# Performance work log

Hardware: AMD Instinct MI355X
Metric: run time of the kernel (lower is better)

## Reference

```python
import jax, jax.numpy as jnp
import numpy as np

D_ATOM, D_PAIR, D_HID = 128, 64, 32
NF, NLOC = 1, 384


def setup_inputs() -> dict:
    key = jax.random.key(0)
    k1, k2, k3, k4, k5 = jax.random.split(key, 5)
    m = jax.random.normal(k1, (NF, NLOC, D_ATOM), dtype=jnp.float32)
    nlist = jax.random.randint(k2, (NF, NLOC, 32), 0, NLOC)
    op_mask = jnp.ones((1,), dtype=jnp.float32)
    op_norm = jnp.ones((1,), dtype=jnp.float32)
    # linear_in: d_atom -> 2*d_hid ; linear_out: d_hid**2 -> d_pair
    W_in = jax.random.normal(k3, (2 * D_HID, D_ATOM), dtype=jnp.float32) * 0.05
    b_in = jnp.zeros((2 * D_HID,), dtype=jnp.float32)
    W_out = jax.random.normal(k4, (D_PAIR, D_HID * D_HID), dtype=jnp.float32) * 0.05
    b_out = jnp.zeros((D_PAIR,), dtype=jnp.float32)
    return {"m": m, "nlist": nlist, "op_mask": op_mask, "op_norm": op_norm,
            "W_in": W_in, "b_in": b_in, "W_out": W_out, "b_out": b_out}


def reference(m, nlist, op_mask, op_norm, W_in, b_in, W_out, b_out):
    # ab: [nf, nloc, 2*d_hid]
    ab = jnp.einsum('fnd,hd->fnh', m, W_in) + b_in
    ab = ab * op_mask
    a, b = jnp.split(ab, 2, axis=-1)  # each [nf, nloc, d_hid]
    nf, nloc, d = a.shape
    # outer product: [nf, nloc, nloc, d_hid*d_hid]
    outer = jnp.einsum('fix,fjy->fijxy', a, b).reshape(nf, nloc, nloc, d * d)
    z = jnp.einsum('fijk,pk->fijp', outer, W_out) + b_out  # [nf, nloc, nloc, d_pair]
    return z * op_norm
```

## Files before the change

kernel.cpp:

```cpp
#include <hip/hip_runtime.h>

#define D_ATOM 128
#define D_PAIR 64
#define D_HID  32
#define NLOC   384


__global__ __launch_bounds__(256) void k_ab(const float* __restrict__ m,
                                            const float* __restrict__ W_in,
                                            const float* __restrict__ b_in,
                                            const float* __restrict__ op_mask,
                                            float* __restrict__ ab) {
    const int t  = threadIdx.x;
    const int h  = t & 63;
    const int ng = __builtin_amdgcn_readfirstlane(t >> 6);
    const int n  = blockIdx.x * 4 + ng;
    const float* mrow = m + n * D_ATOM;
    const float* wrow = W_in + h * D_ATOM;
    float acc = 0.f;
#pragma unroll
    for (int dq = 0; dq < D_ATOM / 4; ++dq) {
        const float4 w  = *reinterpret_cast<const float4*>(wrow + dq * 4);
        const float4 mv = *reinterpret_cast<const float4*>(mrow + dq * 4);
        acc += w.x * mv.x + w.y * mv.y + w.z * mv.z + w.w * mv.w;
    }
    ab[n * 64 + h] = (acc + b_in[h]) * op_mask[0];
}

__global__ __launch_bounds__(256) void k_T(const float* __restrict__ ab,
                                           const float* __restrict__ W_out,
                                           float* __restrict__ T) {
    const int t  = threadIdx.x;
    const int p  = t & 63;
    const int xl = t >> 6;
    const int xt = blockIdx.x & 7;
    const int jt = blockIdx.x >> 3;
    const int x  = xt * 4 + xl;
    float4 w[8];
#pragma unroll
    for (int yq = 0; yq < 8; ++yq)
        w[yq] = *reinterpret_cast<const float4*>(W_out + p * 1024 + x * 32 + yq * 4);
#pragma unroll
    for (int jj = 0; jj < 16; ++jj) {
        const int j = jt * 16 + jj;
        const float* brow = ab + j * 64 + 32;
        float acc = 0.f;
#pragma unroll
        for (int yq = 0; yq < 8; ++yq) {
            const float4 b4 = *reinterpret_cast<const float4*>(brow + yq * 4);
            acc += b4.x * w[yq].x + b4.y * w[yq].y + b4.z * w[yq].z + b4.w * w[yq].w;
        }
        T[j * 2048 + x * 64 + p] = acc;
    }
}

__global__ __launch_bounds__(256) void k_main(const float* __restrict__ ab,
                                              const float* __restrict__ T,
                                              const float* __restrict__ b_out,
                                              const float* __restrict__ op_norm,
                                              float* __restrict__ out) {
    const int t    = threadIdx.x;
    const int p    = t & 63;
    const int wv   = __builtin_amdgcn_readfirstlane(t >> 6);
    const int j    = blockIdx.x >> 1;
    const int half = blockIdx.x & 1;

    float treg[32];
#pragma unroll
    for (int x = 0; x < 32; ++x) treg[x] = T[j * 2048 + x * 64 + p];
    const float bout = b_out[p];
    const float norm = op_norm[0];

    const int ibase = half * 192 + wv * 48;
    for (int c = 0; c < 6; ++c) {
        const int i0 = ibase + c * 8;
        float acc[8];
#pragma unroll
        for (int r = 0; r < 8; ++r) acc[r] = bout;
        const float* arow = ab + i0 * 64;
#pragma unroll
        for (int xq = 0; xq < 8; ++xq) {
#pragma unroll
            for (int r = 0; r < 8; ++r) {
                const float4 av = *reinterpret_cast<const float4*>(arow + r * 64 + xq * 4);
                acc[r] += av.x * treg[xq * 4 + 0] + av.y * treg[xq * 4 + 1] +
                          av.z * treg[xq * 4 + 2] + av.w * treg[xq * 4 + 3];
            }
        }
        float* orow = out + (i0 * NLOC + j) * 64 + p;
#pragma unroll
        for (int r = 0; r < 8; ++r)
            orow[r * NLOC * 64] = acc[r] * norm;
    }
}

extern "C" void kernel_launch(void* const* d_in, const int* in_sizes, int n_in,
                              void* d_out, int out_size, void* d_ws, size_t ws_size,
                              hipStream_t stream) {
    const float* m       = (const float*)d_in[0];
    const float* op_mask = (const float*)d_in[2];
    const float* op_norm = (const float*)d_in[3];
    const float* W_in    = (const float*)d_in[4];
    const float* b_in    = (const float*)d_in[5];
    const float* W_out   = (const float*)d_in[6];
    const float* b_out   = (const float*)d_in[7];
    float* out = (float*)d_out;

    float* ab = (float*)d_ws;
    float* T  = (float*)((char*)d_ws + 98304);

    k_ab  <<<96,  256, 0, stream>>>(m, W_in, b_in, op_mask, ab);
    k_T   <<<192, 256, 0, stream>>>(ab, W_out, T);
    k_main<<<768, 256, 0, stream>>>(ab, T, b_out, op_norm, out);
}
```

Baseline: 106.0 us.

## Fuse ab and T prep kernels; retile main kernel with float4 outputs

Result: slower. 153.7 us (+45.0%).

```diff
diff --git a/kernel.cpp b/kernel.cpp
--- a/kernel.cpp
+++ b/kernel.cpp
@@ -1,96 +1,108 @@
 #include <hip/hip_runtime.h>
 
-#define D_ATOM 128
-#define D_PAIR 64
-#define D_HID  32
-#define NLOC   384
+#define NLOC 384
 
 
-__global__ __launch_bounds__(256) void k_ab(const float* __restrict__ m,
-                                            const float* __restrict__ W_in,
-                                            const float* __restrict__ b_in,
-                                            const float* __restrict__ op_mask,
-                                            float* __restrict__ ab) {
+__global__ __launch_bounds__(256) void k_prep(const float* __restrict__ m,
+                                              const float* __restrict__ W_in,
+                                              const float* __restrict__ b_in,
+                                              const float* __restrict__ op_mask,
+                                              const float* __restrict__ W_out,
+                                              float* __restrict__ ab,
+                                              float* __restrict__ T) {
     const int t  = threadIdx.x;
     const int h  = t & 63;
-    const int ng = __builtin_amdgcn_readfirstlane(t >> 6);
-    const int n  = blockIdx.x * 4 + ng;
-    const float* mrow = m + n * D_ATOM;
-    const float* wrow = W_in + h * D_ATOM;
-    float acc = 0.f;
+    const int rr = __builtin_amdgcn_readfirstlane(t >> 6);
+    const int jb = blockIdx.x * 8;
+    __shared__ float bsh[8][32];
+
+    const float mask = op_mask[0];
+    const float bi   = b_in[h];
+
 #pragma unroll
-    for (int dq = 0; dq < D_ATOM / 4; ++dq) {
-        const float4 w  = *reinterpret_cast<const float4*>(wrow + dq * 4);
-        const float4 mv = *reinterpret_cast<const float4*>(mrow + dq * 4);
-        acc += w.x * mv.x + w.y * mv.y + w.z * mv.z + w.w * mv.w;
-    }
-    ab[n * 64 + h] = (acc + b_in[h]) * op_mask[0];
-}
-
-__global__ __launch_bounds__(256) void k_T(const float* __restrict__ ab,
-                                           const float* __restrict__ W_out,
-                                           float* __restrict__ T) {
-    const int t  = threadIdx.x;
-    const int p  = t & 63;
-    const int xl = t >> 6;
-    const int xt = blockIdx.x & 7;
-    const int jt = blockIdx.x >> 3;
-    const int x  = xt * 4 + xl;
-    float4 w[8];
-#pragma unroll
-    for (int yq = 0; yq < 8; ++yq)
-        w[yq] = *reinterpret_cast<const float4*>(W_out + p * 1024 + x * 32 + yq * 4);
-#pragma unroll
-    for (int jj = 0; jj < 16; ++jj) {
-        const int j = jt * 16 + jj;
-        const float* brow = ab + j * 64 + 32;
+    for (int rg = 0; rg < 2; ++rg) {
+        const int n = jb + rg * 4 + rr;
+        const float* mrow = m + n * 128;
+        const float* wrow = W_in + h * 128;
         float acc = 0.f;
 #pragma unroll
-        for (int yq = 0; yq < 8; ++yq) {
-            const float4 b4 = *reinterpret_cast<const float4*>(brow + yq * 4);
-            acc += b4.x * w[yq].x + b4.y * w[yq].y + b4.z * w[yq].z + b4.w * w[yq].w;
+        for (int q = 0; q < 32; ++q) {
+            const float4 wv = *reinterpret_cast<const float4*>(wrow + q * 4);
+            const float4 mv = *reinterpret_cast<const float4*>(mrow + q * 4);
+            acc += wv.x * mv.x + wv.y * mv.y + wv.z * mv.z + wv.w * mv.w;
         }
-        T[j * 2048 + x * 64 + p] = acc;
+        const float val = (acc + bi) * mask;
+        ab[n * 64 + h] = val;
+        if (h >= 32) bsh[rg * 4 + rr][h - 32] = val;
+    }
+    __syncthreads();
+
+    const int p = h;
+#pragma unroll
+    for (int xs = 0; xs < 8; ++xs) {
+        const int x = rr * 8 + xs;
+        float4 w[8];
+#pragma unroll
+        for (int yq = 0; yq < 8; ++yq)
+            w[yq] = *reinterpret_cast<const float4*>(W_out + p * 1024 + x * 32 + yq * 4);
+#pragma unroll
+        for (int jj = 0; jj < 8; ++jj) {
+            float acc = 0.f;
+#pragma unroll
+            for (int yq = 0; yq < 8; ++yq) {
+                const float4 b4 = *reinterpret_cast<const float4*>(&bsh[jj][yq * 4]);
+                acc += b4.x * w[yq].x + b4.y * w[yq].y + b4.z * w[yq].z + b4.w * w[yq].w;
+            }
+            T[(jb + jj) * 2048 + x * 64 + p] = acc;
+        }
     }
 }
 
-__global__ __launch_bounds__(256) void k_main(const float* __restrict__ ab,
-                                              const float* __restrict__ T,
-                                              const float* __restrict__ b_out,
-                                              const float* __restrict__ op_norm,
-                                              float* __restrict__ out) {
+__global__ __launch_bounds__(256) void k_main2(const float* __restrict__ ab,
+                                               const float* __restrict__ T,
+                                               const float* __restrict__ b_out,
+                                               const float* __restrict__ op_norm,
+                                               float* __restrict__ out) {
     const int t    = threadIdx.x;
-    const int p    = t & 63;
+    const int lane = t & 63;
     const int wv   = __builtin_amdgcn_readfirstlane(t >> 6);
-    const int j    = blockIdx.x >> 1;
-    const int half = blockIdx.x & 1;
+    const int bid  = blockIdx.x;
+    const int jt   = bid % 24;
+    const int it   = bid / 24;
+    const int jq   = lane >> 4;
+    const int p4   = (lane & 15) * 4;
+    const int j    = jt * 16 + wv * 4 + jq;
+    const int i0   = it * 16;
 
-    float treg[32];
-#pragma unroll
-    for (int x = 0; x < 32; ++x) treg[x] = T[j * 2048 + x * 64 + p];
-    const float bout = b_out[p];
+    const float4 bo  = *reinterpret_cast<const float4*>(b_out + p4);
     const float norm = op_norm[0];
 
-    const int ibase = half * 192 + wv * 48;
-    for (int c = 0; c < 6; ++c) {
-        const int i0 = ibase + c * 8;
-        float acc[8];
+    float4 acc[16];
 #pragma unroll
-        for (int r = 0; r < 8; ++r) acc[r] = bout;
-        const float* arow = ab + i0 * 64;
+    for (int i = 0; i < 16; ++i) acc[i] = bo;
+
+    const float* Tj   = T + j * 2048 + p4;
+    const float* arow = ab + i0 * 64;
+
+#pragma unroll 4
+    for (int x = 0; x < 32; ++x) {
+        const float4 t4 = *reinterpret_cast<const float4*>(Tj + x * 64);
 #pragma unroll
-        for (int xq = 0; xq < 8; ++xq) {
+        for (int i = 0; i < 16; ++i) {
+            const float a = arow[i * 64 + x];
+            acc[i].x += a * t4.x;
+            acc[i].y += a * t4.y;
+            acc[i].z += a * t4.z;
+            acc[i].w += a * t4.w;
+        }
+    }
+
 #pragma unroll
-            for (int r = 0; r < 8; ++r) {
-                const float4 av = *reinterpret_cast<const float4*>(arow + r * 64 + xq * 4);
-                acc[r] += av.x * treg[xq * 4 + 0] + av.y * treg[xq * 4 + 1] +
-                          av.z * treg[xq * 4 + 2] + av.w * treg[xq * 4 + 3];
-            }
-        }
-        float* orow = out + (i0 * NLOC + j) * 64 + p;
-#pragma unroll
-        for (int r = 0; r < 8; ++r)
-            orow[r * NLOC * 64] = acc[r] * norm;
+    for (int i = 0; i < 16; ++i) {
+        float4 r;
+        r.x = acc[i].x * norm; r.y = acc[i].y * norm;
+        r.z = acc[i].z * norm; r.w = acc[i].w * norm;
+        *reinterpret_cast<float4*>(out + ((i0 + i) * NLOC + j) * 64 + p4) = r;
     }
 }
 
@@ -109,7 +121,6 @@
     float* ab = (float*)d_ws;
     float* T  = (float*)((char*)d_ws + 98304);
 
-    k_ab  <<<96,  256, 0, stream>>>(m, W_in, b_in, op_mask, ab);
-    k_T   <<<192, 256, 0, stream>>>(ab, W_out, T);
-    k_main<<<768, 256, 0, stream>>>(ab, T, b_out, op_norm, out);
+    k_prep <<<48,  256, 0, stream>>>(m, W_in, b_in, op_mask, W_out, ab, T);
+    k_main2<<<576, 256, 0, stream>>>(ab, T, b_out, op_norm, out);
 }
```
